# Kernel optimization log

Measured on AMD Instinct MI355X. Metric: run time of the kernel, lower is better.

Reference implementation:

```python
import jax, jax.numpy as jnp
import numpy as np

BIG = 1.0e9   # sentinel for masked distances / masked max
K_NBR = 64    # max_num_neighbors in radius()


def _fps(pos, n_sample):
    """Farthest point sampling on a single cloud pos [N, D] -> int32 [n_sample]."""
    n = pos.shape[0]

    def body(i, st):
        d, idxs = st
        last = pos[idxs[i - 1]]                              # [D]
        d = jnp.minimum(d, jnp.sum((pos - last) ** 2, axis=-1))
        return d, idxs.at[i].set(jnp.argmax(d).astype(jnp.int32))

    d0 = jnp.full((n,), BIG, pos.dtype)
    idxs0 = jnp.zeros((n_sample,), jnp.int32)
    _, idxs = jax.lax.fori_loop(1, n_sample, body, (d0, idxs0))
    return idxs


def _mlp2(h, w1, b1, w2, b2):
    # PyG MLP([a,b,c]) in eval mode (dropout off, batch-norm at default running
    # stats == identity): Linear -> ReLU -> Linear (plain last layer).
    return jax.nn.relu(h @ w1 + b1) @ w2 + b2


_gather = jax.vmap(lambda a, i: a[i])  # per-cloud fancy gather


def _sa(x, pos, ratio, r, w1, b1, w2, b2):
    """SAModule: FPS -> radius neighbors (<=K) -> PointConv (gather, MLP on
    [x_j, pos_j - pos_i], max-aggregate). Dense batched: x [B,N,C], pos [B,N,D]."""
    B, N, D = pos.shape
    M = int(round(N * ratio))
    idx = jax.vmap(lambda p: _fps(p, M))(pos)                 # [B, M]
    pos_q = _gather(pos, idx)                                 # [B, M, D]
    # pairwise squared distances query -> all points  [B, M, N]
    d2 = jnp.sum((pos_q[:, :, None, :] - pos[:, None, :, :]) ** 2, axis=-1)
    neg = jnp.where(d2 <= r * r, -d2, -BIG)
    vals, nbr = jax.lax.top_k(neg, K_NBR)                     # [B, M, K]
    valid = vals > -0.5 * BIG                                 # in-radius mask
    x_j = _gather(x, nbr)                                     # [B, M, K, C]
    rel = _gather(pos, nbr) - pos_q[:, :, None, :]            # [B, M, K, D]
    h = _mlp2(jnp.concatenate([x_j, rel], axis=-1), w1, b1, w2, b2)
    h = jnp.where(valid[..., None], h, -BIG)
    return jnp.max(h, axis=2), pos_q                          # max aggregation


def setup_inputs() -> dict:
    key = jax.random.key(0)
    ks = jax.random.split(key, 12)
    B, N, D, F = 8, 4096, 2, 5

    def lin(k, fi, fo):
        return (jax.random.normal(k, (fi, fo), jnp.float32) / np.sqrt(fi)).astype(jnp.float32)

    return {
        "x": jax.random.normal(ks[0], (B, N, F), jnp.float32),
        "pos": jax.random.uniform(ks[1], (B, N, D), jnp.float32),
        # sa1: MLP([5+2, 32, 64])
        "w1a": lin(ks[2], 7, 32),   "b1a": jnp.zeros((32,), jnp.float32),
        "w1b": lin(ks[3], 32, 64),  "b1b": jnp.zeros((64,), jnp.float32),
        # sa2: MLP([64+2, 64, 128])
        "w2a": lin(ks[4], 66, 64),  "b2a": jnp.zeros((64,), jnp.float32),
        "w2b": lin(ks[5], 64, 128), "b2b": jnp.zeros((128,), jnp.float32),
        # sa3 (global): MLP([128+2, 128, 256])
        "w3a": lin(ks[6], 130, 128), "b3a": jnp.zeros((128,), jnp.float32),
        "w3b": lin(ks[7], 128, 256), "b3b": jnp.zeros((256,), jnp.float32),
        # head: MLP([256, 256, 1024], norm=None)
        "w4a": lin(ks[8], 256, 256),  "b4a": jnp.zeros((256,), jnp.float32),
        "w4b": lin(ks[9], 256, 1024), "b4b": jnp.zeros((1024,), jnp.float32),
    }


def reference(x, pos, w1a, b1a, w1b, b1b, w2a, b2a, w2b, b2b,
              w3a, b3a, w3b, b3b, w4a, b4a, w4b, b4b):
    h1, p1 = _sa(x, pos, 0.5, 0.2, w1a, b1a, w1b, b1b)       # [B, N/2, 64]
    h2, p2 = _sa(h1, p1, 0.25, 0.4, w2a, b2a, w2b, b2b)      # [B, N/8, 128]
    g = _mlp2(jnp.concatenate([h2, p2], axis=-1), w3a, b3a, w3b, b3b)
    g = jnp.max(g, axis=1)                                    # global max pool [B, 256]
    return _mlp2(g, w4a, b4a, w4b, b4b)                       # [B, 1024]
```

## Files before the change

### kernel.cpp

```cpp
#include <hip/hip_runtime.h>


#define DPP_UMAX(u, ctrl)                                                      \
  do {                                                                         \
    unsigned _o = (unsigned)__builtin_amdgcn_update_dpp(0, (int)(u), (ctrl),   \
                                                        0xf, 0xf, true);       \
    (u) = ((u) > _o) ? (u) : _o;                                               \
  } while (0)

template<int PPT, int T>
__device__ __forceinline__ void fps_stage(
    float (&xr)[PPT], float (&yr)[PPT], int Msel, int t,
    const float* srcx, const float* srcy,
    float* outx, float* outy,
    unsigned long long* sp ) {
  constexpr int NW = T / 64;
  constexpr int HP = PPT / 2;
  float lx = srcx[0], ly = srcy[0];
  if (t == 0) { outx[0] = lx; outy[0] = ly; }
  float d[PPT];
#pragma unroll
  for (int k = 0; k < PPT; ++k) d[k] = 1e9f;

  for (int i = 1; i < Msel; ++i) {
#pragma unroll
    for (int k = 0; k < PPT; ++k) {
      float dx = xr[k] - lx, dy = yr[k] - ly;
      float dd = __fadd_rn(__fmul_rn(dx, dx), __fmul_rn(dy, dy));
      d[k] = fminf(d[k], dd);
    }
    float bvA = d[0]; int bkA = 0;
    float bvB = d[HP]; int bkB = HP;
#pragma unroll
    for (int k = 1; k < HP; ++k) {
      if (d[k] > bvA)      { bvA = d[k];      bkA = k; }
      if (d[HP + k] > bvB) { bvB = d[HP + k]; bkB = HP + k; }
    }
    float bv = bvA; int bk = bkA;
    if (bvB > bvA) { bv = bvB; bk = bkB; }
    const int bp = t * PPT + bk;
    const unsigned mybits = __float_as_uint(bv);
    unsigned u = mybits;
    DPP_UMAX(u, 0x111);
    DPP_UMAX(u, 0x112);
    DPP_UMAX(u, 0x114);
    DPP_UMAX(u, 0x118);
    DPP_UMAX(u, 0x142);
    DPP_UMAX(u, 0x143);
    const unsigned wvb = (unsigned)__builtin_amdgcn_readlane((int)u, 63);
    const unsigned long long tmask = __ballot(mybits == wvb);
    const int fl = (int)__builtin_ctzll(tmask);
    const int wbp = __builtin_amdgcn_readlane(bp, fl);
    const int par = i & 1;
    if ((t & 63) == 0)
      sp[par * NW + (t >> 6)] =
          ((unsigned long long)wvb << 32) | (unsigned)(~wbp);
    __syncthreads();
    const unsigned long long* sl = &sp[par * NW];
    unsigned long long best = sl[0];
#pragma unroll
    for (int j = 1; j < NW; ++j) {
      unsigned long long v = sl[j];
      best = (v > best) ? v : best;
    }
    const int wi = (int)(~(unsigned)best);
    lx = srcx[wi]; ly = srcy[wi];
    if (t == 0) { outx[i] = lx; outy[i] = ly; }
  }
}

template<int N, int M1, int M2, int T>
__global__ __launch_bounds__(T, 1) void fps_fused_kernel(
    const float* __restrict__ pos,
    float* __restrict__ posq1,
    float* __restrict__ posq2) {
  constexpr int PPT  = N / T;
  constexpr int PPT2 = M1 / T;
  constexpr int NW   = T / 64;
  __shared__ float sx[N], sy[N];
  __shared__ float wlx[M1], wly[M1];
  __shared__ float wl2x[M2], wl2y[M2];
  __shared__ unsigned long long sp[2 * NW];
  const int b = blockIdx.x, t = threadIdx.x;
  float xr[PPT], yr[PPT];
  const float4* p4 = (const float4*)(pos + (size_t)b * N * 2 + (size_t)t * PPT * 2);
#pragma unroll
  for (int q = 0; q < PPT / 2; ++q) {
    float4 v = p4[q];
    xr[2 * q + 0] = v.x; yr[2 * q + 0] = v.y;
    xr[2 * q + 1] = v.z; yr[2 * q + 1] = v.w;
  }
#pragma unroll
  for (int k = 0; k < PPT; ++k) {
    int pt = t * PPT + k;
    sx[pt] = xr[k]; sy[pt] = yr[k];
  }
  __syncthreads();
  fps_stage<PPT, T>(xr, yr, M1, t, sx, sy, wlx, wly, sp);
  __syncthreads();
  for (int j = t; j < M1; j += T)
    ((float2*)posq1)[(size_t)b * M1 + j] = make_float2(wlx[j], wly[j]);
  float x2[PPT2], y2[PPT2];
#pragma unroll
  for (int k = 0; k < PPT2; ++k) { x2[k] = wlx[t * PPT2 + k]; y2[k] = wly[t * PPT2 + k]; }
  fps_stage<PPT2, T>(x2, y2, M2, t, wlx, wly, wl2x, wl2y, sp);
  __syncthreads();
  for (int j = t; j < M2; j += T)
    ((float2*)posq2)[(size_t)b * M2 + j] = make_float2(wl2x[j], wl2y[j]);
}

template<int CPL>
__global__ __launch_bounds__(256) void nbr_kernel(
    const float* __restrict__ pts,
    const float* __restrict__ posq,
    int* __restrict__ nbr,
    int M, int NPTS, int total_q, float R2) {
  const int wid = blockIdx.x * 4 + (threadIdx.x >> 6);
  if (wid >= total_q) return;
  const int lane = threadIdx.x & 63;
  const int b = wid / M;
  const float qx = posq[(size_t)wid * 2 + 0], qy = posq[(size_t)wid * 2 + 1];
  const float* p = pts + (size_t)b * NPTS * 2;
  unsigned bits[CPL];
  int cnt = 0;
#pragma unroll
  for (int k = 0; k < CPL; ++k) {
    int pt = lane + (k << 6);
    float dx = p[pt * 2 + 0] - qx, dy = p[pt * 2 + 1] - qy;
    float dd = __fadd_rn(__fmul_rn(dx, dx), __fmul_rn(dy, dy));
    bool inr = (dd <= R2);
    bits[k] = inr ? __float_as_uint(dd) : 0xFFFFFFFFu;
    cnt += __popcll(__ballot(inr));
  }
  const unsigned long long below = (1ULL << lane) - 1ULL;
  if (cnt <= 64) {
    int base = 0;
#pragma unroll
    for (int k = 0; k < CPL; ++k) {
      bool s = (bits[k] != 0xFFFFFFFFu);
      unsigned long long m = __ballot(s);
      if (s) nbr[(size_t)wid * 64 + base + __popcll(m & below)] = lane + (k << 6);
      base += __popcll(m);
    }
    for (int j = base + lane; j < 64; j += 64) nbr[(size_t)wid * 64 + j] = -1;
  } else {
    unsigned lo = 0, hi = __float_as_uint(R2);
    while (lo < hi) {
      unsigned mid = lo + ((hi - lo) >> 1);
      int c = 0;
#pragma unroll
      for (int k = 0; k < CPL; ++k) c += __popcll(__ballot(bits[k] <= mid));
      if (c >= 64) hi = mid; else lo = mid + 1;
    }
    int cless = 0;
#pragma unroll
    for (int k = 0; k < CPL; ++k) cless += __popcll(__ballot(bits[k] < lo));
    const int need = 64 - cless;
    int base = 0, tiecnt = 0;
#pragma unroll
    for (int k = 0; k < CPL; ++k) {
      bool tie = (bits[k] == lo);
      unsigned long long tm = __ballot(tie);
      bool s = (bits[k] < lo) || (tie && (tiecnt + __popcll(tm & below)) < need);
      tiecnt += __popcll(tm);
      unsigned long long m = __ballot(s);
      if (s) nbr[(size_t)wid * 64 + base + __popcll(m & below)] = lane + (k << 6);
      base += __popcll(m);
    }
  }
}

template<int CIN, int H, int COUT, int QPB, int NPTS, int HS, int W1P>
__global__ __launch_bounds__(64 * QPB) void conv_kernel(
    const float* __restrict__ x,
    const float* __restrict__ pts,
    const float* __restrict__ posq,
    const int* __restrict__ nbr,
    const float* __restrict__ W1, const float* __restrict__ b1,
    const float* __restrict__ W2, const float* __restrict__ b2,
    float* __restrict__ out,
    int M) {
  constexpr int CI2 = CIN + 2;
  __shared__ float sW1t[H * W1P];
  __shared__ float sB1[H];
  __shared__ float sHH[QPB * 64 * HS];
  const int tid = threadIdx.x;
  for (int j = tid; j < CI2 * H; j += 64 * QPB) {
    int c = j / H, h = j - c * H;
    sW1t[h * W1P + c] = W1[j];
  }
  for (int j = tid; j < H; j += 64 * QPB) sB1[j] = b1[j];
  __syncthreads();
  const int wv = tid >> 6, lane = tid & 63;
  const int wid = blockIdx.x * QPB + wv;
  const int b = wid / M;
  const int idx = nbr[(size_t)wid * 64 + lane];
  const unsigned long long vm = __ballot(idx >= 0);
  const int ii = (idx < 0) ? 0 : idx;
  float in[CI2];
  {
    const float* xp = x + ((size_t)b * NPTS + ii) * CIN;
#pragma unroll
    for (int c = 0; c < CIN; ++c) in[c] = xp[c];
    float qx = posq[(size_t)wid * 2 + 0], qy = posq[(size_t)wid * 2 + 1];
    const float* pp = pts + ((size_t)b * NPTS + ii) * 2;
    in[CIN] = pp[0] - qx;
    in[CIN + 1] = pp[1] - qy;
  }
  float* hbase = &sHH[wv * 64 * HS];
#pragma unroll
  for (int h = 0; h < H; h += 4) {
    float vv[4];
#pragma unroll
    for (int j = 0; j < 4; ++j) {
      float a = sB1[h + j];
#pragma unroll
      for (int c = 0; c < CI2; ++c) a = fmaf(in[c], sW1t[(h + j) * W1P + c], a);
      vv[j] = fmaxf(a, 0.0f);
    }
    *(float4*)&hbase[lane * HS + h] = make_float4(vv[0], vv[1], vv[2], vv[3]);
  }
#pragma unroll
  for (int half = 0; half < COUT / 64; ++half) {
    const int o = half * 64 + lane;
    float w2r[H];
#pragma unroll
    for (int h = 0; h < H; ++h) w2r[h] = W2[h * COUT + o];
    const float b2o = b2[o];
    float m = -1e30f;
    for (int n = 0; n < 64; ++n) {
      const float4* hp = (const float4*)&hbase[n * HS];
      float a = b2o;
#pragma unroll
      for (int j = 0; j < H / 4; ++j) {
        float4 hv = hp[j];
        a = fmaf(hv.x, w2r[4 * j + 0], a);
        a = fmaf(hv.y, w2r[4 * j + 1], a);
        a = fmaf(hv.z, w2r[4 * j + 2], a);
        a = fmaf(hv.w, w2r[4 * j + 3], a);
      }
      a = ((vm >> n) & 1ULL) ? a : -1e9f;
      m = fmaxf(m, a);
    }
    out[(size_t)wid * COUT + o] = m;
  }
}

__global__ __launch_bounds__(256) void u_kernel(
    const float* __restrict__ h2,
    const float* __restrict__ posq2,
    const float* __restrict__ W3a, const float* __restrict__ b3a,
    float* __restrict__ u) {
  const int p = blockIdx.x * 2 + (threadIdx.x >> 7);
  const int h = threadIdx.x & 127;
  const float* hp = h2 + (size_t)p * 128;
  float a = b3a[h];
  for (int c = 0; c < 128; ++c) a = fmaf(hp[c], W3a[c * 128 + h], a);
  a = fmaf(posq2[(size_t)p * 2 + 0], W3a[128 * 128 + h], a);
  a = fmaf(posq2[(size_t)p * 2 + 1], W3a[129 * 128 + h], a);
  u[(size_t)p * 128 + h] = fmaxf(a, 0.0f);
}

__global__ __launch_bounds__(256) void g_kernel(
    const float* __restrict__ u,
    const float* __restrict__ W3b, const float* __restrict__ b3b,
    float* __restrict__ part) {
  __shared__ float su[64 * 128];
  const int bb = blockIdx.x;
  const float* up = u + (size_t)bb * 64 * 128;
  for (int j = threadIdx.x; j < 64 * 128; j += 256) su[j] = up[j];
  __syncthreads();
  const int o = threadIdx.x;
  float w[128];
#pragma unroll
  for (int h = 0; h < 128; ++h) w[h] = W3b[h * 256 + o];
  float m = -1e30f;
  for (int p = 0; p < 64; ++p) {
    float a = b3b[o];
    const float4* sp = (const float4*)&su[p * 128];
#pragma unroll
    for (int j = 0; j < 32; ++j) {
      float4 v = sp[j];
      a = fmaf(v.x, w[4 * j + 0], a);
      a = fmaf(v.y, w[4 * j + 1], a);
      a = fmaf(v.z, w[4 * j + 2], a);
      a = fmaf(v.w, w[4 * j + 3], a);
    }
    m = fmaxf(m, a);
  }
  part[(size_t)bb * 256 + o] = m;
}

__global__ __launch_bounds__(256) void head_kernel(
    const float* __restrict__ part,
    const float* __restrict__ W4a, const float* __restrict__ b4a,
    const float* __restrict__ W4b, const float* __restrict__ b4b,
    float* __restrict__ out) {
  __shared__ float g[256], h4[256];
  const int b = blockIdx.x, t = threadIdx.x;
  float m = part[(size_t)(b * 8 + 0) * 256 + t];
  for (int c = 1; c < 8; ++c) m = fmaxf(m, part[(size_t)(b * 8 + c) * 256 + t]);
  g[t] = m;
  __syncthreads();
  float a = b4a[t];
  for (int c = 0; c < 256; ++c) a = fmaf(g[c], W4a[c * 256 + t], a);
  h4[t] = fmaxf(a, 0.0f);
  __syncthreads();
  for (int jj = 0; jj < 4; ++jj) {
    int o = t + jj * 256;
    float a2 = b4b[o];
    for (int c = 0; c < 256; ++c) a2 = fmaf(h4[c], W4b[c * 1024 + o], a2);
    out[(size_t)b * 1024 + o] = a2;
  }
}

extern "C" void kernel_launch(void* const* d_in, const int* in_sizes, int n_in,
                              void* d_out, int out_size, void* d_ws, size_t ws_size,
                              hipStream_t stream) {
  (void)in_sizes; (void)n_in; (void)out_size; (void)ws_size;
  const float* x   = (const float*)d_in[0];
  const float* pos = (const float*)d_in[1];
  const float* w1a = (const float*)d_in[2];  const float* b1a = (const float*)d_in[3];
  const float* w1b = (const float*)d_in[4];  const float* b1b = (const float*)d_in[5];
  const float* w2a = (const float*)d_in[6];  const float* b2a = (const float*)d_in[7];
  const float* w2b = (const float*)d_in[8];  const float* b2b = (const float*)d_in[9];
  const float* w3a = (const float*)d_in[10]; const float* b3a = (const float*)d_in[11];
  const float* w3b = (const float*)d_in[12]; const float* b3b = (const float*)d_in[13];
  const float* w4a = (const float*)d_in[14]; const float* b4a = (const float*)d_in[15];
  const float* w4b = (const float*)d_in[16]; const float* b4b = (const float*)d_in[17];
  float* outp = (float*)d_out;

  char* ws = (char*)d_ws;
  size_t off = 0;
  float* posq1 = (float*)(ws + off); off += (size_t)8 * 2048 * 2 * 4;
  float* posq2 = (float*)(ws + off); off += (size_t)8 * 512 * 2 * 4;
  int*   nbr1  = (int*)  (ws + off); off += (size_t)16384 * 64 * 4;
  int*   nbr2  = (int*)  (ws + off); off += (size_t)4096 * 64 * 4;
  float* h1    = (float*)(ws + off); off += (size_t)16384 * 64 * 4;
  float* h2    = (float*)(ws + off); off += (size_t)4096 * 128 * 4;
  float* u3    = (float*)(ws + off); off += (size_t)4096 * 128 * 4;
  float* part  = (float*)(ws + off); off += (size_t)64 * 256 * 4;

  fps_fused_kernel<4096, 2048, 512, 512><<<dim3(8), dim3(512), 0, stream>>>(
      pos, posq1, posq2);
  nbr_kernel<64><<<dim3(4096), dim3(256), 0, stream>>>(pos, posq1, nbr1,
                                                       2048, 4096, 16384, 0.04f);
  conv_kernel<5, 32, 64, 4, 4096, 36, 8><<<dim3(4096), dim3(256), 0, stream>>>(
      x, pos, posq1, nbr1, w1a, b1a, w1b, b1b, h1, 2048);
  nbr_kernel<32><<<dim3(1024), dim3(256), 0, stream>>>(posq1, posq2, nbr2,
                                                       512, 2048, 4096, 0.16f);
  conv_kernel<64, 64, 128, 2, 2048, 68, 68><<<dim3(2048), dim3(128), 0, stream>>>(
      h1, posq1, posq2, nbr2, w2a, b2a, w2b, b2b, h2, 512);
  u_kernel<<<dim3(2048), dim3(256), 0, stream>>>(h2, posq2, w3a, b3a, u3);
  g_kernel<<<dim3(64), dim3(256), 0, stream>>>(u3, w3b, b3b, part);
  head_kernel<<<dim3(8), dim3(256), 0, stream>>>(part, w4a, b4a, w4b, b4b, outp);
}
```

Baseline: 2.022 ms.

## Overlap second FPS stage with fused stage-1 neighbor search and conv

Replaces the FPS kernel plus the stage-1 neighbor and conv kernels with one cooperative kernel. Eight blocks run FPS; after a grid sync, those blocks run the second FPS stage while the other 248 blocks run the stage-1 radius search and PointConv, fused per query with neighbor indices kept in shared memory. This hides the serial second FPS behind the stage-1 conv work and removes the nbr1 buffer round trip. The cost is fewer blocks for the conv work, a 64-entry per-thread bits array that may spill registers, and reliance on cooperative launch residency.

```diff
diff --git a/kernel.cpp b/kernel.cpp
--- a/kernel.cpp
+++ b/kernel.cpp
@@ -1,4 +1,7 @@
 #include <hip/hip_runtime.h>
+#include <hip/hip_cooperative_groups.h>
+
+namespace cg = cooperative_groups;
 
 
 #define DPP_UMAX(u, ctrl)                                                      \
@@ -69,52 +72,192 @@
   }
 }
 
-template<int N, int M1, int M2, int T>
-__global__ __launch_bounds__(T, 1) void fps_fused_kernel(
+__global__ __launch_bounds__(512) void mega_kernel(
     const float* __restrict__ pos,
+    const float* __restrict__ xin,
     float* __restrict__ posq1,
-    float* __restrict__ posq2) {
-  constexpr int PPT  = N / T;
-  constexpr int PPT2 = M1 / T;
-  constexpr int NW   = T / 64;
-  __shared__ float sx[N], sy[N];
-  __shared__ float wlx[M1], wly[M1];
-  __shared__ float wl2x[M2], wl2y[M2];
-  __shared__ unsigned long long sp[2 * NW];
-  const int b = blockIdx.x, t = threadIdx.x;
+    float* __restrict__ posq2,
+    float* __restrict__ h1,
+    const float* __restrict__ W1, const float* __restrict__ B1,
+    const float* __restrict__ W2, const float* __restrict__ B2)
+{
+  constexpr int N = 4096, M1 = 2048, M2 = 512, T = 512;
+  constexpr int PPT = N / T, PPT2 = M1 / T, NW = T / 64;
+  constexpr int H = 32, CI2 = 7, HS = 36, W1P = 8;
+  __shared__ union {
+    struct {
+      float sx[N], sy[N];
+      float wlx[M1], wly[M1];
+      float wl2x[M2], wl2y[M2];
+      unsigned long long sp[2 * NW];
+    } f;
+    struct {
+      float sW1t[H * W1P];
+      float sB1[H];
+      float sHH[8 * 64 * HS];
+      int   sNbr[8][64];
+    } c;
+  } sh;
+  const int bid = blockIdx.x, t = threadIdx.x;
+  cg::grid_group grid = cg::this_grid();
+
   float xr[PPT], yr[PPT];
-  const float4* p4 = (const float4*)(pos + (size_t)b * N * 2 + (size_t)t * PPT * 2);
-#pragma unroll
-  for (int q = 0; q < PPT / 2; ++q) {
-    float4 v = p4[q];
-    xr[2 * q + 0] = v.x; yr[2 * q + 0] = v.y;
-    xr[2 * q + 1] = v.z; yr[2 * q + 1] = v.w;
-  }
-#pragma unroll
-  for (int k = 0; k < PPT; ++k) {
-    int pt = t * PPT + k;
-    sx[pt] = xr[k]; sy[pt] = yr[k];
-  }
-  __syncthreads();
-  fps_stage<PPT, T>(xr, yr, M1, t, sx, sy, wlx, wly, sp);
-  __syncthreads();
-  for (int j = t; j < M1; j += T)
-    ((float2*)posq1)[(size_t)b * M1 + j] = make_float2(wlx[j], wly[j]);
-  float x2[PPT2], y2[PPT2];
-#pragma unroll
-  for (int k = 0; k < PPT2; ++k) { x2[k] = wlx[t * PPT2 + k]; y2[k] = wly[t * PPT2 + k]; }
-  fps_stage<PPT2, T>(x2, y2, M2, t, wlx, wly, wl2x, wl2y, sp);
-  __syncthreads();
-  for (int j = t; j < M2; j += T)
-    ((float2*)posq2)[(size_t)b * M2 + j] = make_float2(wl2x[j], wl2y[j]);
+  if (bid < 8) {
+    const int b = bid;
+    const float4* p4 =
+        (const float4*)(pos + (size_t)b * N * 2 + (size_t)t * PPT * 2);
+#pragma unroll
+    for (int q = 0; q < PPT / 2; ++q) {
+      float4 v = p4[q];
+      xr[2 * q + 0] = v.x; yr[2 * q + 0] = v.y;
+      xr[2 * q + 1] = v.z; yr[2 * q + 1] = v.w;
+    }
+#pragma unroll
+    for (int k = 0; k < PPT; ++k) {
+      int pt = t * PPT + k;
+      sh.f.sx[pt] = xr[k]; sh.f.sy[pt] = yr[k];
+    }
+    __syncthreads();
+    fps_stage<PPT, T>(xr, yr, M1, t, sh.f.sx, sh.f.sy, sh.f.wlx, sh.f.wly,
+                      sh.f.sp);
+    __syncthreads();
+    for (int j = t; j < M1; j += T)
+      ((float2*)posq1)[(size_t)b * M1 + j] =
+          make_float2(sh.f.wlx[j], sh.f.wly[j]);
+    __threadfence();
+  }
+  grid.sync();
+
+  if (bid < 8) {
+    const int b = bid;
+    float x2[PPT2], y2[PPT2];
+#pragma unroll
+    for (int k = 0; k < PPT2; ++k) {
+      x2[k] = sh.f.wlx[t * PPT2 + k];
+      y2[k] = sh.f.wly[t * PPT2 + k];
+    }
+    fps_stage<PPT2, T>(x2, y2, M2, t, sh.f.wlx, sh.f.wly, sh.f.wl2x, sh.f.wl2y,
+                       sh.f.sp);
+    __syncthreads();
+    for (int j = t; j < M2; j += T)
+      ((float2*)posq2)[(size_t)b * M2 + j] =
+          make_float2(sh.f.wl2x[j], sh.f.wl2y[j]);
+  } else {
+    for (int j = t; j < CI2 * H; j += T) {
+      int cc = j / H, hh = j - cc * H;
+      sh.c.sW1t[hh * W1P + cc] = W1[j];
+    }
+    for (int j = t; j < H; j += T) sh.c.sB1[j] = B1[j];
+    __syncthreads();
+    const int wv = t >> 6, lane = t & 63;
+    const unsigned long long below = (1ULL << lane) - 1ULL;
+    float* hbase = &sh.c.sHH[wv * 64 * HS];
+    int* snb = sh.c.sNbr[wv];
+    for (int wid = (bid - 8) * 8 + wv; wid < 16384; wid += 248 * 8) {
+      const int b = wid >> 11;
+      const float qx = posq1[2 * wid + 0], qy = posq1[2 * wid + 1];
+      const float* p = pos + (size_t)b * N * 2;
+      snb[lane] = -1;
+      unsigned bits[64];
+      int cnt = 0;
+#pragma unroll
+      for (int k = 0; k < 64; ++k) {
+        int pt = lane + (k << 6);
+        float dx = p[pt * 2 + 0] - qx, dy = p[pt * 2 + 1] - qy;
+        float dd = __fadd_rn(__fmul_rn(dx, dx), __fmul_rn(dy, dy));
+        bool inr = (dd <= 0.04f);
+        bits[k] = inr ? __float_as_uint(dd) : 0xFFFFFFFFu;
+        cnt += __popcll(__ballot(inr));
+      }
+      if (cnt <= 64) {
+        int base = 0;
+#pragma unroll
+        for (int k = 0; k < 64; ++k) {
+          bool s = (bits[k] != 0xFFFFFFFFu);
+          unsigned long long m = __ballot(s);
+          if (s) snb[base + __popcll(m & below)] = lane + (k << 6);
+          base += __popcll(m);
+        }
+      } else {
+        unsigned lo = 0, hi = __float_as_uint(0.04f);
+        while (lo < hi) {
+          unsigned mid = lo + ((hi - lo) >> 1);
+          int c = 0;
+#pragma unroll
+          for (int k = 0; k < 64; ++k) c += __popcll(__ballot(bits[k] <= mid));
+          if (c >= 64) hi = mid; else lo = mid + 1;
+        }
+        int cless = 0;
+#pragma unroll
+        for (int k = 0; k < 64; ++k) cless += __popcll(__ballot(bits[k] < lo));
+        const int need = 64 - cless;
+        int base = 0, tiecnt = 0;
+#pragma unroll
+        for (int k = 0; k < 64; ++k) {
+          bool tie = (bits[k] == lo);
+          unsigned long long tm = __ballot(tie);
+          bool s = (bits[k] < lo) ||
+                   (tie && (tiecnt + __popcll(tm & below)) < need);
+          tiecnt += __popcll(tm);
+          unsigned long long m = __ballot(s);
+          if (s) snb[base + __popcll(m & below)] = lane + (k << 6);
+          base += __popcll(m);
+        }
+      }
+      const int idx = snb[lane];
+      const unsigned long long vm = __ballot(idx >= 0);
+      const int ii = (idx < 0) ? 0 : idx;
+      float in[CI2];
+      {
+        const float* xp = xin + ((size_t)b * N + ii) * 5;
+#pragma unroll
+        for (int c = 0; c < 5; ++c) in[c] = xp[c];
+        const float* pp = p + (size_t)ii * 2;
+        in[5] = pp[0] - qx;
+        in[6] = pp[1] - qy;
+      }
+#pragma unroll
+      for (int h = 0; h < H; h += 4) {
+        float vv[4];
+#pragma unroll
+        for (int j = 0; j < 4; ++j) {
+          float a = sh.c.sB1[h + j];
+#pragma unroll
+          for (int c = 0; c < CI2; ++c)
+            a = fmaf(in[c], sh.c.sW1t[(h + j) * W1P + c], a);
+          vv[j] = fmaxf(a, 0.0f);
+        }
+        *(float4*)&hbase[lane * HS + h] = make_float4(vv[0], vv[1], vv[2], vv[3]);
+      }
+      const int o = lane;
+      float w2r[H];
+#pragma unroll
+      for (int h = 0; h < H; ++h) w2r[h] = W2[h * 64 + o];
+      const float b2o = B2[o];
+      float m = -1e30f;
+      for (int n = 0; n < 64; ++n) {
+        const float4* hp = (const float4*)&hbase[n * HS];
+        float a = b2o;
+#pragma unroll
+        for (int j = 0; j < H / 4; ++j) {
+          float4 hv = hp[j];
+          a = fmaf(hv.x, w2r[4 * j + 0], a);
+          a = fmaf(hv.y, w2r[4 * j + 1], a);
+          a = fmaf(hv.z, w2r[4 * j + 2], a);
+          a = fmaf(hv.w, w2r[4 * j + 3], a);
+        }
+        a = ((vm >> n) & 1ULL) ? a : -1e9f;
+        m = fmaxf(m, a);
+      }
+      h1[(size_t)wid * 64 + o] = m;
+    }
+  }
 }
 
 template<int CPL>
 __global__ __launch_bounds__(256) void nbr_kernel(
-    const float* __restrict__ pts,
-    const float* __restrict__ posq,
-    int* __restrict__ nbr,
-    int M, int NPTS, int total_q, float R2) {
+    const float* __restrict__ pts, const float* __restrict__ posq,
+    int* __restrict__ nbr, int M, int NPTS, int total_q, float R2) {
   const int wid = blockIdx.x * 4 + (threadIdx.x >> 6);
   if (wid >= total_q) return;
   const int lane = threadIdx.x & 63;
@@ -172,14 +315,11 @@
 
 template<int CIN, int H, int COUT, int QPB, int NPTS, int HS, int W1P>
 __global__ __launch_bounds__(64 * QPB) void conv_kernel(
-    const float* __restrict__ x,
-    const float* __restrict__ pts,
-    const float* __restrict__ posq,
-    const int* __restrict__ nbr,
+    const float* __restrict__ x, const float* __restrict__ pts,
+    const float* __restrict__ posq, const int* __restrict__ nbr,
     const float* __restrict__ W1, const float* __restrict__ b1,
     const float* __restrict__ W2, const float* __restrict__ b2,
-    float* __restrict__ out,
-    int M) {
+    float* __restrict__ out, int M) {
   constexpr int CI2 = CIN + 2;
   __shared__ float sW1t[H * W1P];
   __shared__ float sB1[H];
@@ -247,8 +387,7 @@
 }
 
 __global__ __launch_bounds__(256) void u_kernel(
-    const float* __restrict__ h2,
-    const float* __restrict__ posq2,
+    const float* __restrict__ h2, const float* __restrict__ posq2,
     const float* __restrict__ W3a, const float* __restrict__ b3a,
     float* __restrict__ u) {
   const int p = blockIdx.x * 2 + (threadIdx.x >> 7);
@@ -262,9 +401,8 @@
 }
 
 __global__ __launch_bounds__(256) void g_kernel(
-    const float* __restrict__ u,
-    const float* __restrict__ W3b, const float* __restrict__ b3b,
-    float* __restrict__ part) {
+    const float* __restrict__ u, const float* __restrict__ W3b,
+    const float* __restrict__ b3b, float* __restrict__ part) {
   __shared__ float su[64 * 128];
   const int bb = blockIdx.x;
   const float* up = u + (size_t)bb * 64 * 128;
@@ -292,10 +430,9 @@
 }
 
 __global__ __launch_bounds__(256) void head_kernel(
-    const float* __restrict__ part,
-    const float* __restrict__ W4a, const float* __restrict__ b4a,
-    const float* __restrict__ W4b, const float* __restrict__ b4b,
-    float* __restrict__ out) {
+    const float* __restrict__ part, const float* __restrict__ W4a,
+    const float* __restrict__ b4a, const float* __restrict__ W4b,
+    const float* __restrict__ b4b, float* __restrict__ out) {
   __shared__ float g[256], h4[256];
   const int b = blockIdx.x, t = threadIdx.x;
   float m = part[(size_t)(b * 8 + 0) * 256 + t];
@@ -334,19 +471,17 @@
   size_t off = 0;
   float* posq1 = (float*)(ws + off); off += (size_t)8 * 2048 * 2 * 4;
   float* posq2 = (float*)(ws + off); off += (size_t)8 * 512 * 2 * 4;
-  int*   nbr1  = (int*)  (ws + off); off += (size_t)16384 * 64 * 4;
   int*   nbr2  = (int*)  (ws + off); off += (size_t)4096 * 64 * 4;
   float* h1    = (float*)(ws + off); off += (size_t)16384 * 64 * 4;
   float* h2    = (float*)(ws + off); off += (size_t)4096 * 128 * 4;
   float* u3    = (float*)(ws + off); off += (size_t)4096 * 128 * 4;
   float* part  = (float*)(ws + off); off += (size_t)64 * 256 * 4;
 
-  fps_fused_kernel<4096, 2048, 512, 512><<<dim3(8), dim3(512), 0, stream>>>(
-      pos, posq1, posq2);
-  nbr_kernel<64><<<dim3(4096), dim3(256), 0, stream>>>(pos, posq1, nbr1,
-                                                       2048, 4096, 16384, 0.04f);
-  conv_kernel<5, 32, 64, 4, 4096, 36, 8><<<dim3(4096), dim3(256), 0, stream>>>(
-      x, pos, posq1, nbr1, w1a, b1a, w1b, b1b, h1, 2048);
+  void* kargs[] = {(void*)&pos, (void*)&x, (void*)&posq1, (void*)&posq2,
+                   (void*)&h1, (void*)&w1a, (void*)&b1a, (void*)&w1b,
+                   (void*)&b1b};
+  hipLaunchCooperativeKernel((void*)mega_kernel, dim3(256), dim3(512), kargs,
+                             0, stream);
   nbr_kernel<32><<<dim3(1024), dim3(256), 0, stream>>>(posq1, posq2, nbr2,
                                                        512, 2048, 4096, 0.16f);
   conv_kernel<64, 64, 128, 2, 2048, 68, 68><<<dim3(2048), dim3(128), 0, stream>>>(
```

Result: no change. 2.001 ms (-1.0%).
